# Performance work log

Measured on AMD Instinct MI355X. Metric: run time of the kernel, lower is better.

The kernel has to match this reference:

```python
import jax, jax.numpy as jnp
import numpy as np

DECAY = 0.1
EPS = 1e-5


def setup_inputs() -> dict:
    key = jax.random.key(0)
    k1, k2, k3, k4 = jax.random.split(key, 4)
    N, K, D = 262144, 1024, 64
    x = jax.random.normal(k1, (N, D), dtype=jnp.float32)
    embed = jax.random.normal(k2, (K, D), dtype=jnp.float32) * 0.01
    cluster_size = jax.random.uniform(k3, (K,), dtype=jnp.float32)
    embed_avg = jax.random.normal(k4, (K, D), dtype=jnp.float32) * 0.01
    return {"x": x, "embed": embed, "cluster_size": cluster_size, "embed_avg": embed_avg}


def reference(x, embed, cluster_size, embed_avg):
    # x: [N, D] flattened latents; embed: [K, D] codebook
    N, D = x.shape
    K = embed.shape[0]

    # Squared Euclidean distance (same argmin as torch.cdist p=2).
    x2 = jnp.sum(x * x, axis=-1, keepdims=True)            # [N, 1]
    e2 = jnp.sum(embed * embed, axis=-1)                   # [K]
    dist = x2 - 2.0 * jnp.einsum('nd,kd->nk', x, embed) + e2[None, :]  # [N, K]
    embed_ind = jnp.argmin(dist, axis=-1)                  # [N] int

    # Quantize: gather nearest codes.
    quantize = embed[embed_ind]                            # [N, D]

    # --- EMA codebook update (no-grad in the original) ---
    xs = jax.lax.stop_gradient(x)
    bins = jax.ops.segment_sum(jnp.ones((N,), dtype=x.dtype), embed_ind,
                               num_segments=K)             # [K] bincount
    embed_sum = jax.ops.segment_sum(xs, embed_ind, num_segments=K)  # [K, D] scatter-add

    cluster_size_new = cluster_size * DECAY + bins * (1.0 - DECAY)
    embed_avg_new = embed_avg * DECAY + embed_sum * (1.0 - DECAY)

    # Laplace smoothing then normalize to get the updated codebook.
    n = jnp.sum(cluster_size_new)
    cs_smoothed = (cluster_size_new + EPS) / (n + K * EPS) * n
    embed_normalized = embed_avg_new / cs_smoothed[:, None]  # [K, D]

    return quantize, embed_ind, cluster_size_new, embed_avg_new, embed_normalized
```

## Files before the change

### kernel.cpp

```cpp
#include <hip/hip_runtime.h>
#include <hip/hip_bf16.h>


#define NROWS 262144
#define KCODES 1024
#define DDIM 64
#define CAPL 8

typedef __attribute__((ext_vector_type(8)))  short short8;
typedef __attribute__((ext_vector_type(16))) float f32x16;

__device__ __forceinline__ unsigned short f2bf(float f) {
    unsigned u = __float_as_uint(f);
    unsigned r = u + 0x7fffu + ((u >> 16) & 1u);
    return (unsigned short)(r >> 16);
}

__global__ __launch_bounds__(256) void vq_prep(
    const float* __restrict__ embed, unsigned short* __restrict__ eb,
    float* __restrict__ e2f, float* __restrict__ enmax2)
{
    const int k = blockIdx.x * 256 + threadIdx.x;
    const float* er = embed + (size_t)k * DDIM;
    float s = 0.f;
    #pragma unroll
    for (int d = 0; d < DDIM; ++d) { float v = er[d]; s = fmaf(v, v, s); }
    e2f[k] = s;
    #pragma unroll
    for (int d = 0; d < DDIM; ++d) eb[(size_t)k * DDIM + d] = f2bf(er[d]);
    atomicMax((int*)enmax2, __float_as_int(s));
}

__global__ __launch_bounds__(512, 4) void vq_phaseA(
    const float* __restrict__ x, const unsigned short* __restrict__ eb,
    const float* __restrict__ e2f, const float* __restrict__ enmax2,
    float* __restrict__ out_ind, int* __restrict__ candg, int* __restrict__ cntg,
    int* __restrict__ wl, int* __restrict__ gcount,
    int* __restrict__ wl2, int* __restrict__ gcount2)
{
    __shared__ __align__(16) unsigned short ebs[8 * 32 * 64];
    __shared__ float norm2L[256];
    __shared__ int   cntL[256];
    __shared__ int   candL[256][CAPL];
    __shared__ int   mcount, mbase, mcount2, mbase2;

    const int t    = threadIdx.x;
    const int lane = t & 63;
    const int wid  = t >> 6;
    const int lo   = lane & 31;
    const int hi   = lane >> 5;
    const int rowb = blockIdx.x * 256;
    const int myrow = rowb + wid * 32 + lo;

    short8 af[4];
    float xsq = 0.f;
    {
        const float* xr = x + (size_t)myrow * DDIM;
        #pragma unroll
        for (int i = 0; i < 4; ++i) {
            const float4 a = *reinterpret_cast<const float4*>(xr + 16 * i + 8 * hi);
            const float4 b = *reinterpret_cast<const float4*>(xr + 16 * i + 8 * hi + 4);
            short8 f;
            f[0] = (short)f2bf(a.x); f[1] = (short)f2bf(a.y);
            f[2] = (short)f2bf(a.z); f[3] = (short)f2bf(a.w);
            f[4] = (short)f2bf(b.x); f[5] = (short)f2bf(b.y);
            f[6] = (short)f2bf(b.z); f[7] = (short)f2bf(b.w);
            af[i] = f;
            xsq = fmaf(a.x, a.x, xsq); xsq = fmaf(a.y, a.y, xsq);
            xsq = fmaf(a.z, a.z, xsq); xsq = fmaf(a.w, a.w, xsq);
            xsq = fmaf(b.x, b.x, xsq); xsq = fmaf(b.y, b.y, xsq);
            xsq = fmaf(b.z, b.z, xsq); xsq = fmaf(b.w, b.w, xsq);
        }
    }
    const float n2full = xsq + __shfl_xor(xsq, 32);
    if (hi == 0) norm2L[wid * 32 + lo] = n2full;
    if (t < 256) cntL[t] = 0;
    if (t == 0) { mcount = 0; mcount2 = 0; }
    const float en2 = *enmax2;

    f32x16 best;
    #pragma unroll
    for (int r = 0; r < 16; ++r) best[r] = 3.4e38f;

    for (int p = 0; p < 4; ++p) {
        __syncthreads();
        #pragma unroll
        for (int it = 0; it < 4; ++it) {
            const int f16  = t + it * 512;
            const int ch8  = f16 >> 8;
            const int r    = f16 & 255;
            const int code = r >> 3, slot = r & 7;
            const short8 v = *reinterpret_cast<const short8*>(eb + (size_t)p * 16384 + f16 * 8);
            *reinterpret_cast<short8*>((char*)ebs + ch8 * 4096 + code * 128 +
                                       ((slot ^ (code & 7)) << 4)) = v;
        }
        __syncthreads();
        for (int c8 = 0; c8 < 8; ++c8) {
            const int ch = p * 8 + c8;
            short8 bfr[4];
            #pragma unroll
            for (int i = 0; i < 4; ++i) {
                const int slot = 2 * i + hi;
                bfr[i] = *reinterpret_cast<const short8*>(
                    (char*)ebs + c8 * 4096 + lo * 128 + (((slot ^ (lo & 7))) << 4));
            }
            const float e2l = e2f[ch * 32 + lo];
            f32x16 acc;
            #pragma unroll
            for (int r = 0; r < 16; ++r) acc[r] = 0.f;
            #pragma unroll
            for (int i = 0; i < 4; ++i)
                acc = __builtin_amdgcn_mfma_f32_32x32x16_bf16(af[i], bfr[i], acc, 0, 0, 0);
            #pragma unroll
            for (int r = 0; r < 16; ++r)
                best[r] = fminf(best[r], fmaf(-2.f, acc[r], e2l));
        }
    }

    #pragma unroll
    for (int r = 0; r < 16; ++r) {
        float v = best[r];
        v = fminf(v, __shfl_xor(v, 1));  v = fminf(v, __shfl_xor(v, 2));
        v = fminf(v, __shfl_xor(v, 4));  v = fminf(v, __shfl_xor(v, 8));
        v = fminf(v, __shfl_xor(v, 16));
        const int rr = (r & 3) + 8 * (r >> 2) + 4 * hi;
        const float nr2 = norm2L[wid * 32 + rr];
        best[r] = v + 0.015625f * sqrtf(nr2 * en2) + 1e-4f;
    }

    for (int p = 0; p < 4; ++p) {
        __syncthreads();
        #pragma unroll
        for (int it = 0; it < 4; ++it) {
            const int f16  = t + it * 512;
            const int ch8  = f16 >> 8;
            const int r    = f16 & 255;
            const int code = r >> 3, slot = r & 7;
            const short8 v = *reinterpret_cast<const short8*>(eb + (size_t)p * 16384 + f16 * 8);
            *reinterpret_cast<short8*>((char*)ebs + ch8 * 4096 + code * 128 +
                                       ((slot ^ (code & 7)) << 4)) = v;
        }
        __syncthreads();
        for (int c8 = 0; c8 < 8; ++c8) {
            const int ch = p * 8 + c8;
            short8 bfr[4];
            #pragma unroll
            for (int i = 0; i < 4; ++i) {
                const int slot = 2 * i + hi;
                bfr[i] = *reinterpret_cast<const short8*>(
                    (char*)ebs + c8 * 4096 + lo * 128 + (((slot ^ (lo & 7))) << 4));
            }
            const float e2l = e2f[ch * 32 + lo];
            f32x16 acc;
            #pragma unroll
            for (int r = 0; r < 16; ++r) acc[r] = 0.f;
            #pragma unroll
            for (int i = 0; i < 4; ++i)
                acc = __builtin_amdgcn_mfma_f32_32x32x16_bf16(af[i], bfr[i], acc, 0, 0, 0);
            #pragma unroll
            for (int r = 0; r < 16; ++r) {
                const float d0 = fmaf(-2.f, acc[r], e2l);
                if (d0 <= best[r]) {
                    const int rr = (r & 3) + 8 * (r >> 2) + 4 * hi;
                    const int rl = wid * 32 + rr;
                    const int idx = atomicAdd(&cntL[rl], 1);
                    if (idx < CAPL) candL[rl][idx] = ch * 32 + lo;
                }
            }
        }
    }
    __syncthreads();

    int my = -1, my2 = -1, c = 0;
    if (t < 256) {
        c = cntL[t];
        if (c == 1)           out_ind[rowb + t] = (float)candL[t][0];
        else if (c <= CAPL)   my  = atomicAdd(&mcount, 1);
        else                  my2 = atomicAdd(&mcount2, 1);
    }
    __syncthreads();
    if (t == 0) { mbase = atomicAdd(gcount, mcount); mbase2 = atomicAdd(gcount2, mcount2); }
    __syncthreads();
    if (my >= 0) {
        const int row = rowb + t;
        wl[mbase + my] = row;
        cntg[row] = c;
        #pragma unroll
        for (int j = 0; j < CAPL; ++j)
            if (j < c) candg[row * 8 + j] = candL[t][j];
    }
    if (my2 >= 0) wl2[mbase2 + my2] = rowb + t;
}

__global__ __launch_bounds__(256) void vq_rerank1(
    const float* __restrict__ x, const float* __restrict__ embed,
    const float* __restrict__ e2f, const int* __restrict__ wl,
    const int* __restrict__ gcount, const int* __restrict__ cntg,
    const int* __restrict__ candg, float* __restrict__ out_ind)
{
    const int n = *gcount;
    for (int i = blockIdx.x * 256 + threadIdx.x; i < n; i += gridDim.x * 256) {
        const int row = wl[i];
        float xv[DDIM];
        {
            const float4* xp = reinterpret_cast<const float4*>(x + (size_t)row * DDIM);
            float4 xq[16];
            #pragma unroll
            for (int q = 0; q < 16; ++q) xq[q] = xp[q];
            #pragma unroll
            for (int q = 0; q < 16; ++q) {
                xv[q*4+0] = xq[q].x; xv[q*4+1] = xq[q].y;
                xv[q*4+2] = xq[q].z; xv[q*4+3] = xq[q].w;
            }
        }
        float x2 = 0.f;
        #pragma unroll
        for (int d = 0; d < DDIM; ++d) x2 = fmaf(xv[d], xv[d], x2);

        const int c = cntg[row];
        float bv = 3.4e38f; int bk = 0x7fffffff;
        for (int ci = 0; ci < c; ++ci) {
            const int k = candg[row * 8 + ci];
            const float4* ep = reinterpret_cast<const float4*>(embed + (size_t)k * DDIM);
            float dot = 0.f;
            #pragma unroll
            for (int q = 0; q < 16; ++q) {
                const float4 e4 = ep[q];
                dot = fmaf(xv[q*4+0], e4.x, dot);
                dot = fmaf(xv[q*4+1], e4.y, dot);
                dot = fmaf(xv[q*4+2], e4.z, dot);
                dot = fmaf(xv[q*4+3], e4.w, dot);
            }
            const float dist = (x2 - 2.0f * dot) + e2f[k];
            if (dist < bv || (dist == bv && k < bk)) { bv = dist; bk = k; }
        }
        out_ind[row] = (float)bk;
    }
}

__global__ __launch_bounds__(256) void vq_rerank2(
    const float* __restrict__ x, const float* __restrict__ embed,
    const float* __restrict__ e2f, const int* __restrict__ wl2,
    const int* __restrict__ gcount2, float* __restrict__ out_ind)
{
    const int t    = threadIdx.x;
    const int lane = t & 63;
    const int gw   = (blockIdx.x * 256 + t) >> 6;
    const int nw   = (gridDim.x * 256) >> 6;
    const int n    = *gcount2;

    for (int e = gw; e < n; e += nw) {
        const int row = wl2[e];
        float xv[DDIM];
        {
            const float4* xp = reinterpret_cast<const float4*>(x + (size_t)row * DDIM);
            #pragma unroll
            for (int q = 0; q < 16; ++q) {
                const float4 v = xp[q];
                xv[q*4+0] = v.x; xv[q*4+1] = v.y; xv[q*4+2] = v.z; xv[q*4+3] = v.w;
            }
        }
        float x2 = 0.f;
        #pragma unroll
        for (int d = 0; d < DDIM; ++d) x2 = fmaf(xv[d], xv[d], x2);

        float bv = 3.4e38f; int bk = 0x7fffffff;
        for (int k = lane; k < KCODES; k += 64) {
            const float* er = embed + (size_t)k * DDIM;
            float dot = 0.f;
            #pragma unroll
            for (int d = 0; d < DDIM; ++d) dot = fmaf(xv[d], er[d], dot);
            const float dist = (x2 - 2.0f * dot) + e2f[k];
            if (dist < bv) { bv = dist; bk = k; }
        }
        #pragma unroll
        for (int s = 1; s < 64; s <<= 1) {
            const float ov = __shfl_xor(bv, s);
            const int   ok = __shfl_xor(bk, s);
            if (ov < bv || (ov == bv && ok < bk)) { bv = ov; bk = ok; }
        }
        if (lane == 0) out_ind[row] = (float)bk;
    }
}

__global__ __launch_bounds__(256) void vq_hist(
    const float* __restrict__ out_ind, int* __restrict__ bins_i)
{
    __shared__ int h[KCODES];
    const int t = threadIdx.x;
    #pragma unroll
    for (int j = 0; j < 4; ++j) h[t + 256 * j] = 0;
    __syncthreads();
    const int row = blockIdx.x * 256 + t;
    atomicAdd(&h[(int)out_ind[row]], 1);
    __syncthreads();
    #pragma unroll
    for (int j = 0; j < 4; ++j) {
        const int v = h[t + 256 * j];
        if (v) atomicAdd(bins_i + t + 256 * j, v);
    }
}

__global__ __launch_bounds__(1024) void vq_prefix(
    const int* __restrict__ bins_i, int* __restrict__ offs, int* __restrict__ cursor)
{
    __shared__ int s[KCODES];
    const int t = threadIdx.x;
    const int b = bins_i[t];
    s[t] = b;
    __syncthreads();
    for (int d = 1; d < KCODES; d <<= 1) {
        const int v = (t >= d) ? s[t - d] : 0;
        __syncthreads();
        s[t] += v;
        __syncthreads();
    }
    const int excl = s[t] - b;
    offs[t] = excl;
    cursor[t] = excl;
}

__global__ __launch_bounds__(256) void vq_scatter(
    const float* __restrict__ out_ind, int* __restrict__ cursor, int* __restrict__ sorted)
{
    const int row  = blockIdx.x * 256 + threadIdx.x;
    const int code = (int)out_ind[row];
    const int pos  = atomicAdd(cursor + code, 1);
    sorted[pos] = (code << 20) | row;
}

__global__ __launch_bounds__(256) void vq_reduce(
    const float* __restrict__ x, const int* __restrict__ sorted,
    float* __restrict__ esum)
{
    const int t = threadIdx.x, lane = t & 63, w = t >> 6;
    const int p0 = (blockIdx.x * 4 + w) * 64;

    int cur = sorted[p0] >> 20;
    float acc = 0.f;
    #pragma unroll 4
    for (int i = 0; i < 64; i += 4) {
        const int4 e4 = *reinterpret_cast<const int4*>(sorted + p0 + i);
        const float v0 = x[(size_t)(e4.x & 0xFFFFF) * DDIM + lane];
        const float v1 = x[(size_t)(e4.y & 0xFFFFF) * DDIM + lane];
        const float v2 = x[(size_t)(e4.z & 0xFFFFF) * DDIM + lane];
        const float v3 = x[(size_t)(e4.w & 0xFFFFF) * DDIM + lane];
        const int c0 = e4.x >> 20, c1 = e4.y >> 20, c2 = e4.z >> 20, c3 = e4.w >> 20;
        if (c0 != cur) { unsafeAtomicAdd(esum + cur * DDIM + lane, acc); acc = 0.f; cur = c0; }
        acc += v0;
        if (c1 != cur) { unsafeAtomicAdd(esum + cur * DDIM + lane, acc); acc = 0.f; cur = c1; }
        acc += v1;
        if (c2 != cur) { unsafeAtomicAdd(esum + cur * DDIM + lane, acc); acc = 0.f; cur = c2; }
        acc += v2;
        if (c3 != cur) { unsafeAtomicAdd(esum + cur * DDIM + lane, acc); acc = 0.f; cur = c3; }
        acc += v3;
    }
    unsafeAtomicAdd(esum + cur * DDIM + lane, acc);
}

__global__ __launch_bounds__(1024) void vq_finalize(
    const float* __restrict__ cluster_size, const float* __restrict__ embed_avg,
    const int* __restrict__ bins_i, float* __restrict__ out_cs,
    float* __restrict__ out_eavg, float* __restrict__ out_enorm)
{
    __shared__ float red[KCODES];
    __shared__ float css[KCODES];
    const int t = threadIdx.x;

    const float csn = cluster_size[t] * 0.1f + (float)bins_i[t] * 0.9f;
    red[t] = csn;
    __syncthreads();
    for (int s = 512; s > 0; s >>= 1) {
        if (t < s) red[t] += red[t + s];
        __syncthreads();
    }
    const float n = red[0];
    out_cs[t] = csn;
    css[t] = (csn + 1e-5f) / (n + (float)(KCODES * 1e-5)) * n;
    __syncthreads();

    #pragma unroll
    for (int i = 0; i < 16; ++i) {
        const int f4 = t + i * 1024;
        const int k  = f4 >> 4;
        const float4 ea = reinterpret_cast<const float4*>(embed_avg)[f4];
        const float4 su = reinterpret_cast<const float4*>(out_eavg)[f4];
        const float  cc = css[k];
        float4 ean, en;
        ean.x = ea.x * 0.1f + su.x * 0.9f; en.x = ean.x / cc;
        ean.y = ea.y * 0.1f + su.y * 0.9f; en.y = ean.y / cc;
        ean.z = ea.z * 0.1f + su.z * 0.9f; en.z = ean.z / cc;
        ean.w = ea.w * 0.1f + su.w * 0.9f; en.w = ean.w / cc;
        reinterpret_cast<float4*>(out_eavg)[f4]  = ean;
        reinterpret_cast<float4*>(out_enorm)[f4] = en;
    }
}

__global__ __launch_bounds__(256) void vq_quant(
    const float* __restrict__ out_ind, const float* __restrict__ embed,
    float* __restrict__ out_q)
{
    __shared__ int inds[256];
    const int t = threadIdx.x;
    const int row0 = blockIdx.x * 256;
    inds[t] = (int)out_ind[row0 + t];
    __syncthreads();
    #pragma unroll
    for (int i = 0; i < 16; ++i) {
        const int f = t + i * 256;
        const int r = f >> 4, dq = f & 15;
        const int code = inds[r];
        const float4 ev = *reinterpret_cast<const float4*>(
            embed + (size_t)code * DDIM + dq * 4);
        *reinterpret_cast<float4*>(out_q + (size_t)(row0 + r) * DDIM + dq * 4) = ev;
    }
}

extern "C" void kernel_launch(void* const* d_in, const int* in_sizes, int n_in,
                              void* d_out, int out_size, void* d_ws, size_t ws_size,
                              hipStream_t stream)
{
    const float* x            = (const float*)d_in[0];
    const float* embed        = (const float*)d_in[1];
    const float* cluster_size = (const float*)d_in[2];
    const float* embed_avg    = (const float*)d_in[3];

    float* out      = (float*)d_out;
    float* out_q    = out;
    float* out_ind  = out_q + (size_t)NROWS * DDIM;
    float* out_cs   = out_ind + NROWS;
    float* out_eavg = out_cs + KCODES;
    float* out_en   = out_eavg + (size_t)KCODES * DDIM;

    unsigned short* eb = (unsigned short*)out_en;
    float* e2f    = out_en + 32768;
    float* enmax2 = out_en + 32768 + KCODES;

    int* S      = (int*)out_q;
    int* candg  = S;
    int* cntg   = S + 2097152;
    int* wl     = S + 2359296;
    int* wl2    = S + 2621440;
    int* sorted = S + 2883584;
    int* bins_i = S + 3145728;
    int* offs   = bins_i + KCODES;
    int* cursor = offs + KCODES;
    int* gcount = cursor + KCODES;
    int* gcount2= gcount + 1;

    hipMemsetAsync(bins_i, 0, (3 * KCODES + 2) * sizeof(int), stream);
    hipMemsetAsync(out_eavg, 0, (size_t)KCODES * DDIM * sizeof(float), stream);
    hipMemsetAsync(enmax2, 0, sizeof(float), stream);

    vq_prep    <<<KCODES / 256, 256, 0, stream>>>(embed, eb, e2f, enmax2);
    vq_phaseA  <<<NROWS / 256, 512, 0, stream>>>(x, eb, e2f, enmax2, out_ind,
                                                 candg, cntg, wl, gcount, wl2, gcount2);
    vq_rerank1 <<<1024, 256, 0, stream>>>(x, embed, e2f, wl, gcount, cntg, candg, out_ind);
    vq_rerank2 <<<128, 256, 0, stream>>>(x, embed, e2f, wl2, gcount2, out_ind);
    vq_hist    <<<NROWS / 256, 256, 0, stream>>>(out_ind, bins_i);
    vq_prefix  <<<1, 1024, 0, stream>>>(bins_i, offs, cursor);
    vq_scatter <<<NROWS / 256, 256, 0, stream>>>(out_ind, cursor, sorted);
    vq_reduce  <<<NROWS / 256, 256, 0, stream>>>(x, sorted, out_eavg);
    vq_finalize<<<1, 1024, 0, stream>>>(cluster_size, embed_avg, bins_i,
                                        out_cs, out_eavg, out_en);
    vq_quant   <<<NROWS / 256, 256, 0, stream>>>(out_ind, embed, out_q);
}
```

Baseline: 295.2 us.

## Load full bf16 codebook into LDS once and fold histogram into argmin kernels

```diff
diff --git a/kernel.cpp b/kernel.cpp
--- a/kernel.cpp
+++ b/kernel.cpp
@@ -31,17 +31,17 @@
     atomicMax((int*)enmax2, __float_as_int(s));
 }
 
-__global__ __launch_bounds__(512, 4) void vq_phaseA(
+__global__ __launch_bounds__(1024, 4) void vq_phaseA(
     const float* __restrict__ x, const unsigned short* __restrict__ eb,
     const float* __restrict__ e2f, const float* __restrict__ enmax2,
     float* __restrict__ out_ind, int* __restrict__ candg, int* __restrict__ cntg,
     int* __restrict__ wl, int* __restrict__ gcount,
-    int* __restrict__ wl2, int* __restrict__ gcount2)
-{
-    __shared__ __align__(16) unsigned short ebs[8 * 32 * 64];
-    __shared__ float norm2L[256];
-    __shared__ int   cntL[256];
-    __shared__ int   candL[256][CAPL];
+    int* __restrict__ wl2, int* __restrict__ gcount2, int* __restrict__ bins_i)
+{
+    __shared__ __align__(16) unsigned short ebs[65536];
+    __shared__ float norm2L[512];
+    __shared__ int   cntL[512];
+    __shared__ int   candL[512][CAPL];
     __shared__ int   mcount, mbase, mcount2, mbase2;
 
     const int t    = threadIdx.x;
@@ -49,7 +49,7 @@
     const int wid  = t >> 6;
     const int lo   = lane & 31;
     const int hi   = lane >> 5;
-    const int rowb = blockIdx.x * 256;
+    const int rowb = blockIdx.x * 512;
     const int myrow = rowb + wid * 32 + lo;
 
     short8 af[4];
@@ -74,47 +74,44 @@
     }
     const float n2full = xsq + __shfl_xor(xsq, 32);
     if (hi == 0) norm2L[wid * 32 + lo] = n2full;
-    if (t < 256) cntL[t] = 0;
+
+    #pragma unroll
+    for (int it = 0; it < 8; ++it) {
+        const int f16  = t + it * 1024;
+        const int ch   = f16 >> 8;
+        const int r    = f16 & 255;
+        const int code = r >> 3, slot = r & 7;
+        const short8 v = *reinterpret_cast<const short8*>(eb + (size_t)f16 * 8);
+        *reinterpret_cast<short8*>((char*)ebs + ch * 4096 + code * 128 +
+                                   ((slot ^ (code & 7)) << 4)) = v;
+    }
+    if (t < 512) cntL[t] = 0;
     if (t == 0) { mcount = 0; mcount2 = 0; }
     const float en2 = *enmax2;
+    __syncthreads();
 
     f32x16 best;
     #pragma unroll
     for (int r = 0; r < 16; ++r) best[r] = 3.4e38f;
 
-    for (int p = 0; p < 4; ++p) {
-        __syncthreads();
-        #pragma unroll
-        for (int it = 0; it < 4; ++it) {
-            const int f16  = t + it * 512;
-            const int ch8  = f16 >> 8;
-            const int r    = f16 & 255;
-            const int code = r >> 3, slot = r & 7;
-            const short8 v = *reinterpret_cast<const short8*>(eb + (size_t)p * 16384 + f16 * 8);
-            *reinterpret_cast<short8*>((char*)ebs + ch8 * 4096 + code * 128 +
-                                       ((slot ^ (code & 7)) << 4)) = v;
-        }
-        __syncthreads();
-        for (int c8 = 0; c8 < 8; ++c8) {
-            const int ch = p * 8 + c8;
-            short8 bfr[4];
-            #pragma unroll
-            for (int i = 0; i < 4; ++i) {
-                const int slot = 2 * i + hi;
-                bfr[i] = *reinterpret_cast<const short8*>(
-                    (char*)ebs + c8 * 4096 + lo * 128 + (((slot ^ (lo & 7))) << 4));
-            }
-            const float e2l = e2f[ch * 32 + lo];
-            f32x16 acc;
-            #pragma unroll
-            for (int r = 0; r < 16; ++r) acc[r] = 0.f;
-            #pragma unroll
-            for (int i = 0; i < 4; ++i)
-                acc = __builtin_amdgcn_mfma_f32_32x32x16_bf16(af[i], bfr[i], acc, 0, 0, 0);
-            #pragma unroll
-            for (int r = 0; r < 16; ++r)
-                best[r] = fminf(best[r], fmaf(-2.f, acc[r], e2l));
-        }
+    for (int ch = 0; ch < 32; ++ch) {
+        short8 bfr[4];
+        #pragma unroll
+        for (int i = 0; i < 4; ++i) {
+            const int slot = 2 * i + hi;
+            bfr[i] = *reinterpret_cast<const short8*>(
+                (char*)ebs + ch * 4096 + lo * 128 + (((slot ^ (lo & 7))) << 4));
+        }
+        const float e2l = e2f[ch * 32 + lo];
+        f32x16 acc;
+        #pragma unroll
+        for (int r = 0; r < 16; ++r) acc[r] = 0.f;
+        #pragma unroll
+        for (int i = 0; i < 4; ++i)
+            acc = __builtin_amdgcn_mfma_f32_32x32x16_bf16(af[i], bfr[i], acc, 0, 0, 0);
+        #pragma unroll
+        for (int r = 0; r < 16; ++r)
+            best[r] = fminf(best[r], fmaf(-2.f, acc[r], e2l));
     }
 
     #pragma unroll
@@ -128,53 +125,42 @@
         best[r] = v + 0.015625f * sqrtf(nr2 * en2) + 1e-4f;
     }
 
-    for (int p = 0; p < 4; ++p) {
-        __syncthreads();
-        #pragma unroll
-        for (int it = 0; it < 4; ++it) {
-            const int f16  = t + it * 512;
-            const int ch8  = f16 >> 8;
-            const int r    = f16 & 255;
-            const int code = r >> 3, slot = r & 7;
-            const short8 v = *reinterpret_cast<const short8*>(eb + (size_t)p * 16384 + f16 * 8);
-            *reinterpret_cast<short8*>((char*)ebs + ch8 * 4096 + code * 128 +
-                                       ((slot ^ (code & 7)) << 4)) = v;
-        }
-        __syncthreads();
-        for (int c8 = 0; c8 < 8; ++c8) {
-            const int ch = p * 8 + c8;
-            short8 bfr[4];
-            #pragma unroll
-            for (int i = 0; i < 4; ++i) {
-                const int slot = 2 * i + hi;
-                bfr[i] = *reinterpret_cast<const short8*>(
-                    (char*)ebs + c8 * 4096 + lo * 128 + (((slot ^ (lo & 7))) << 4));
+    for (int ch = 0; ch < 32; ++ch) {
+        short8 bfr[4];
+        #pragma unroll
+        for (int i = 0; i < 4; ++i) {
+            const int slot = 2 * i + hi;
+            bfr[i] = *reinterpret_cast<const short8*>(
+                (char*)ebs + ch * 4096 + lo * 128 + (((slot ^ (lo & 7))) << 4));
+        }
+        const float e2l = e2f[ch * 32 + lo];
+        f32x16 acc;
+        #pragma unroll
+        for (int r = 0; r < 16; ++r) acc[r] = 0.f;
+        #pragma unroll
+        for (int i = 0; i < 4; ++i)
+            acc = __builtin_amdgcn_mfma_f32_32x32x16_bf16(af[i], bfr[i], acc, 0, 0, 0);
+        #pragma unroll
+        for (int r = 0; r < 16; ++r) {
+            const float d0 = fmaf(-2.f, acc[r], e2l);
+            if (d0 <= best[r]) {
+                const int rr = (r & 3) + 8 * (r >> 2) + 4 * hi;
+                const int rl = wid * 32 + rr;
+                const int idx = atomicAdd(&cntL[rl], 1);
+                if (idx < CAPL) candL[rl][idx] = ch * 32 + lo;
             }
-            const float e2l = e2f[ch * 32 + lo];
-            f32x16 acc;
-            #pragma unroll
-            for (int r = 0; r < 16; ++r) acc[r] = 0.f;
-            #pragma unroll
-            for (int i = 0; i < 4; ++i)
-                acc = __builtin_amdgcn_mfma_f32_32x32x16_bf16(af[i], bfr[i], acc, 0, 0, 0);
-            #pragma unroll
-            for (int r = 0; r < 16; ++r) {
-                const float d0 = fmaf(-2.f, acc[r], e2l);
-                if (d0 <= best[r]) {
-                    const int rr = (r & 3) + 8 * (r >> 2) + 4 * hi;
-                    const int rl = wid * 32 + rr;
-                    const int idx = atomicAdd(&cntL[rl], 1);
-                    if (idx < CAPL) candL[rl][idx] = ch * 32 + lo;
-                }
-            }
         }
     }
     __syncthreads();
 
     int my = -1, my2 = -1, c = 0;
-    if (t < 256) {
+    if (t < 512) {
         c = cntL[t];
-        if (c == 1)           out_ind[rowb + t] = (float)candL[t][0];
+        if (c == 1) {
+            const int code = candL[t][0];
+            out_ind[rowb + t] = (float)code;
+            atomicAdd(bins_i + code, 1);
+        }
         else if (c <= CAPL)   my  = atomicAdd(&mcount, 1);
         else                  my2 = atomicAdd(&mcount2, 1);
     }
@@ -196,7 +182,8 @@
     const float* __restrict__ x, const float* __restrict__ embed,
     const float* __restrict__ e2f, const int* __restrict__ wl,
     const int* __restrict__ gcount, const int* __restrict__ cntg,
-    const int* __restrict__ candg, float* __restrict__ out_ind)
+    const int* __restrict__ candg, float* __restrict__ out_ind,
+    int* __restrict__ bins_i)
 {
     const int n = *gcount;
     for (int i = blockIdx.x * 256 + threadIdx.x; i < n; i += gridDim.x * 256) {
@@ -235,13 +222,15 @@
             if (dist < bv || (dist == bv && k < bk)) { bv = dist; bk = k; }
         }
         out_ind[row] = (float)bk;
+        atomicAdd(bins_i + bk, 1);
     }
 }
 
 __global__ __launch_bounds__(256) void vq_rerank2(
     const float* __restrict__ x, const float* __restrict__ embed,
     const float* __restrict__ e2f, const int* __restrict__ wl2,
-    const int* __restrict__ gcount2, float* __restrict__ out_ind)
+    const int* __restrict__ gcount2, float* __restrict__ out_ind,
+    int* __restrict__ bins_i)
 {
     const int t    = threadIdx.x;
     const int lane = t & 63;
@@ -279,25 +268,7 @@
             const int   ok = __shfl_xor(bk, s);
             if (ov < bv || (ov == bv && ok < bk)) { bv = ov; bk = ok; }
         }
-        if (lane == 0) out_ind[row] = (float)bk;
-    }
-}
-
-__global__ __launch_bounds__(256) void vq_hist(
-    const float* __restrict__ out_ind, int* __restrict__ bins_i)
-{
-    __shared__ int h[KCODES];
-    const int t = threadIdx.x;
-    #pragma unroll
-    for (int j = 0; j < 4; ++j) h[t + 256 * j] = 0;
-    __syncthreads();
-    const int row = blockIdx.x * 256 + t;
-    atomicAdd(&h[(int)out_ind[row]], 1);
-    __syncthreads();
-    #pragma unroll
-    for (int j = 0; j < 4; ++j) {
-        const int v = h[t + 256 * j];
-        if (v) atomicAdd(bins_i + t + 256 * j, v);
+        if (lane == 0) { out_ind[row] = (float)bk; atomicAdd(bins_i + bk, 1); }
     }
 }
 
@@ -433,8 +404,7 @@
     float* out_en   = out_eavg + (size_t)KCODES * DDIM;
 
     unsigned short* eb = (unsigned short*)out_en;
-    float* e2f    = out_en + 32768;
-    float* enmax2 = out_en + 32768 + KCODES;
+    float* e2f = out_en + 32768;
 
     int* S      = (int*)out_q;
     int* candg  = S;
@@ -443,21 +413,22 @@
     int* wl2    = S + 2621440;
     int* sorted = S + 2883584;
     int* bins_i = S + 3145728;
-    int* offs   = bins_i + KCODES;
+    int* gcount = bins_i + KCODES;
+    int* gcount2= gcount + 1;
+    float* enmax2 = (float*)(gcount2 + 1);
+    int* offs   = gcount2 + 2;
     int* cursor = offs + KCODES;
-    int* gcount = cursor + KCODES;
-    int* gcount2= gcount + 1;
-
-    hipMemsetAsync(bins_i, 0, (3 * KCODES + 2) * sizeof(int), stream);
+
+    hipMemsetAsync(bins_i, 0, (KCODES + 3) * sizeof(int), stream);
     hipMemsetAsync(out_eavg, 0, (size_t)KCODES * DDIM * sizeof(float), stream);
-    hipMemsetAsync(enmax2, 0, sizeof(float), stream);
 
     vq_prep    <<<KCODES / 256, 256, 0, stream>>>(embed, eb, e2f, enmax2);
-    vq_phaseA  <<<NROWS / 256, 512, 0, stream>>>(x, eb, e2f, enmax2, out_ind,
-                                                 candg, cntg, wl, gcount, wl2, gcount2);
-    vq_rerank1 <<<1024, 256, 0, stream>>>(x, embed, e2f, wl, gcount, cntg, candg, out_ind);
-    vq_rerank2 <<<128, 256, 0, stream>>>(x, embed, e2f, wl2, gcount2, out_ind);
-    vq_hist    <<<NROWS / 256, 256, 0, stream>>>(out_ind, bins_i);
+    vq_phaseA  <<<NROWS / 512, 1024, 0, stream>>>(x, eb, e2f, enmax2, out_ind,
+                                                  candg, cntg, wl, gcount,
+                                                  wl2, gcount2, bins_i);
+    vq_rerank1 <<<512, 256, 0, stream>>>(x, embed, e2f, wl, gcount, cntg, candg,
+                                         out_ind, bins_i);
+    vq_rerank2 <<<128, 256, 0, stream>>>(x, embed, e2f, wl2, gcount2, out_ind, bins_i);
     vq_prefix  <<<1, 1024, 0, stream>>>(bins_i, offs, cursor);
     vq_scatter <<<NROWS / 256, 256, 0, stream>>>(out_ind, cursor, sorted);
     vq_reduce  <<<NROWS / 256, 256, 0, stream>>>(x, sorted, out_eavg);
```

Result: slower. 307.5 us (+4.1%).
